# Kernel tuning notes

Measured on AMD Instinct MI355X. Metric: run time of the kernel, lower is better.

## Reference

```python
import jax, jax.numpy as jnp
import numpy as np

HEAD_DIM = 128
SCALE = 1.0 / np.sqrt(HEAD_DIM).astype(np.float32)


def setup_inputs() -> dict:
    key = jax.random.key(0)
    kq, kk, kv = jax.random.split(key, 3)
    B, S, H, KVH, D = 2, 2048, 32, 8, HEAD_DIM
    q = jax.random.normal(kq, (B, S, H, D), dtype=jnp.float32)
    k = jax.random.normal(kk, (B, S, KVH, D), dtype=jnp.float32)
    v = jax.random.normal(kv, (B, S, KVH, D), dtype=jnp.float32)
    return {"q": q, "k": k, "v": v}


def reference(q, k, v):
    # q: [B,S,H,D]; k,v: [B,S,KVH,D]
    B, S, H, D = q.shape
    kvh = k.shape[2]
    if kvh != H:
        rep = H // kvh
        # repeat_interleave along head dim (GQA -> MHA expansion)
        k = jnp.repeat(k, rep, axis=2)
        v = jnp.repeat(v, rep, axis=2)
    # scores: [B,H,S,S]
    scores = jnp.einsum("bqhd,bkhd->bhqk", q, k) * SCALE
    causal_mask = jnp.triu(jnp.ones((S, S), dtype=bool), k=1)
    scores = jnp.where(causal_mask, -jnp.inf, scores)
    attn = jax.nn.softmax(scores, axis=-1)
    # output back to [B,S,H,D]
    out = jnp.einsum("bhqk,bkhd->bqhd", attn, v)
    return out
```

## Files before the change

kernel.cpp:

```cpp
#include <hip/hip_runtime.h>
#include <hip/hip_bf16.h>
#include <stdint.h>

#define B_    2
#define S_    2048
#define H_    32
#define KVH_  8
#define D_    128
#define NBLK  256
#define NTOT_ 34

typedef __bf16 bf16x8 __attribute__((ext_vector_type(8)));
typedef unsigned short u16x8 __attribute__((ext_vector_type(8)));
typedef unsigned int u32x4 __attribute__((ext_vector_type(4)));
typedef float f32x16 __attribute__((ext_vector_type(16)));

__device__ constexpr float SCALE_LOG2E = 0.08838834764831845f * 1.4426950408889634f;

__device__ __forceinline__ unsigned short f2bf(float f) {
    unsigned int u = __builtin_bit_cast(unsigned int, f);
    u = (u + 0x7FFFu + ((u >> 16) & 1u)) >> 16;
    return (unsigned short)u;
}

__device__ __forceinline__ unsigned int cvt_pk_bf16(float lo, float hi) {
    unsigned int r;
    asm("v_cvt_pk_bf16_f32 %0, %1, %2" : "=v"(r) : "v"(lo), "v"(hi));
    return r;
}

__device__ __forceinline__ void gload16(const unsigned short* gsrc, unsigned short* ldst) {
    __builtin_amdgcn_global_load_lds(
        (const __attribute__((address_space(1))) unsigned int*)gsrc,
        (__attribute__((address_space(3))) unsigned int*)ldst,
        16, 0, 0);
}

__global__ __launch_bounds__(256) void prepass(const float* __restrict__ k,
                                               const float* __restrict__ v,
                                               unsigned short* __restrict__ kbuf,
                                               unsigned short* __restrict__ vbuf) {
    if (blockIdx.x < 1024) {
        __shared__ float tile[32][133];
        int bid = blockIdx.x;
        int kt  = bid & 63;
        int kvh = (bid >> 6) & 7;
        int b   = bid >> 9;
        int t   = threadIdx.x;

        #pragma unroll
        for (int i = 0; i < 4; ++i) {
            int idx = t + 256 * i;
            int r   = idx >> 5;
            int d4  = (idx & 31) * 4;
            float4 x = *(const float4*)(k + (((size_t)b * S_ + kt * 32 + r) * KVH_ + kvh) * D_ + d4);
            tile[r][d4 + 0] = x.x; tile[r][d4 + 1] = x.y;
            tile[r][d4 + 2] = x.z; tile[r][d4 + 3] = x.w;
        }
        __syncthreads();

        #pragma unroll
        for (int i = 0; i < 2; ++i) {
            int s2 = t + 256 * i;
            int ch = s2 >> 6;
            int l  = s2 & 63;
            int row = l & 31, d0 = ch * 16 + (l >> 5) * 8;
            u16x8 o;
            #pragma unroll
            for (int j = 0; j < 8; ++j) o[j] = f2bf(tile[row][d0 + j]);
            *(u16x8*)(kbuf + ((size_t)(((b * KVH_ + kvh) * 64 + kt) * 8 + ch) * 512 + l * 8)) = o;
        }
    } else {
        __shared__ float tile[64][132];
        int bid = blockIdx.x - 1024;
        int u   = bid & 31;
        int kvh = (bid >> 5) & 7;
        int b   = bid >> 8;
        int t   = threadIdx.x;

        int s  = t >> 2;
        int cb = (t & 3) * 32;
        const float* src = v + (((size_t)b * S_ + u * 64 + s) * KVH_ + kvh) * D_ + cb;
        #pragma unroll
        for (int i = 0; i < 8; ++i) {
            float4 x = ((const float4*)src)[i];
            tile[s][cb + 4 * i + 0] = x.x; tile[s][cb + 4 * i + 1] = x.y;
            tile[s][cb + 4 * i + 2] = x.z; tile[s][cb + 4 * i + 3] = x.w;
        }
        __syncthreads();

        #pragma unroll
        for (int i = 0; i < 4; ++i) {
            int slot = t + 256 * i;
            int ci = slot >> 6;
            int l  = slot & 63;
            int kk = ci >> 2, dt = ci & 3;
            int h2 = l >> 5;
            u16x8 o;
            #pragma unroll
            for (int j = 0; j < 8; ++j)
                o[j] = f2bf(tile[kk * 16 + h2 * 8 + j][dt * 32 + (l & 31)]);
            *(u16x8*)(vbuf + ((size_t)(((b * KVH_ + kvh) * 32 + u) * 16 + ci) * 512 + l * 8)) = o;
        }
    }
}

__global__ __launch_bounds__(512, 2)
void attn_fwd(const float* __restrict__ q,
              const unsigned short* __restrict__ kbuf,
              const unsigned short* __restrict__ vbuf,
              float* __restrict__ out)
{
    int pid = blockIdx.x;
    int lid = (pid & 7) * (NBLK / 8) + (pid >> 3);
    int p    = lid & 7;
    int hp   = (lid >> 3) & 1;
    int bkvh = lid >> 4;
    int b    = bkvh >> 3, kvh = bkvh & 7;
    const int qtA = 15 - p;
    const int NTA = 2 * qtA + 2;
    const int qtB = p;

    const int tid = threadIdx.x, wave = tid >> 6, lane = tid & 63;
    const int cw = wave & 3;
    const int h  = kvh * 4 + hp * 2 + (wave >> 2);
    const int c32 = lane & 31, hi = lane >> 5;

    __shared__ __align__(16) unsigned short ldsK[2][8192];
    __shared__ __align__(16) unsigned short ldsV[2][8192];

    const unsigned short* kfb = kbuf + (size_t)(b * KVH_ + kvh) * (S_ * D_);
    const unsigned short* vfb = vbuf + (size_t)(b * KVH_ + kvh) * (S_ * D_);

    auto kvt = [&](int u) { return (u < NTA) ? u : (u - NTA); };
    auto stageK = [&](int u) {
        const unsigned short* ks = kfb + (size_t)kvt(u) * 8192;
        unsigned short* ld = &ldsK[u & 1][0];
        #pragma unroll
        for (int i = 0; i < 2; ++i) {
            int seg = wave * 2 + i;
            gload16(ks + seg * 512 + lane * 8, ld + seg * 512);
        }
    };
    auto stageV = [&](int u) {
        const unsigned short* vs = vfb + (size_t)kvt(u) * 8192;
        unsigned short* ld = &ldsV[u & 1][0];
        #pragma unroll
        for (int i = 0; i < 2; ++i) {
            int seg = wave * 2 + i;
            gload16(vs + seg * 512 + lane * 8, ld + seg * 512);
        }
    };

    stageK(0);
    asm volatile("s_waitcnt vmcnt(0)" ::: "memory");
    __builtin_amdgcn_s_barrier();
    asm volatile("" ::: "memory");

    auto run_tile = [&](int qt, int u0, int NT) {
        const int q0w = qt * 128 + cw * 32;

        bf16x8 qf[8];
        {
            const float* qp = q + ((size_t)b * S_ + q0w + c32) * (H_ * D_) + h * D_ + hi * 8;
            #pragma unroll
            for (int ch = 0; ch < 8; ++ch) {
                float4 a  = ((const float4*)(qp + ch * 16))[0];
                float4 bb = ((const float4*)(qp + ch * 16))[1];
                u16x8 tt;
                tt[0] = f2bf(a.x * SCALE_LOG2E);  tt[1] = f2bf(a.y * SCALE_LOG2E);
                tt[2] = f2bf(a.z * SCALE_LOG2E);  tt[3] = f2bf(a.w * SCALE_LOG2E);
                tt[4] = f2bf(bb.x * SCALE_LOG2E); tt[5] = f2bf(bb.y * SCALE_LOG2E);
                tt[6] = f2bf(bb.z * SCALE_LOG2E); tt[7] = f2bf(bb.w * SCALE_LOG2E);
                qf[ch] = __builtin_bit_cast(bf16x8, tt);
            }
        }

        f32x16 acc[4];
        #pragma unroll
        for (int dt = 0; dt < 4; ++dt)
            #pragma unroll
            for (int i = 0; i < 16; ++i) acc[dt][i] = 0.f;
        float lsum = 0.f;

        u32x4 pfA[4], pfB[4];

        auto body = [&](int u, int it, int NT_, u32x4 (&pfW)[4], u32x4 (&pfR)[4], int ODD) {
            if (u + 1 < NTOT_) stageK(u + 1);
            stageV(u);
            const int k0 = it * 64;
            const bool act  = (k0 <= q0w + 31);
            const bool pact = (it > 0) && (k0 - 64 <= q0w + 31);
            f32x16 sv[2];

            if (act) {
                #pragma unroll
                for (int kt = 0; kt < 2; ++kt)
                    #pragma unroll
                    for (int i = 0; i < 16; ++i) sv[kt][i] = 0.f;
                __builtin_amdgcn_s_setprio(1);
                #pragma unroll
                for (int ch = 0; ch < 8; ++ch) {
                    bf16x8 kf0 = *(const bf16x8*)&ldsK[ODD][(0 * 8 + ch) * 512 + lane * 8];
                    bf16x8 kf1 = *(const bf16x8*)&ldsK[ODD][(1 * 8 + ch) * 512 + lane * 8];
                    sv[0] = __builtin_amdgcn_mfma_f32_32x32x16_bf16(kf0, qf[ch], sv[0], 0, 0, 0);
                    sv[1] = __builtin_amdgcn_mfma_f32_32x32x16_bf16(kf1, qf[ch], sv[1], 0, 0, 0);
                }
                __builtin_amdgcn_s_setprio(0);
            }

            if (pact) {
                __builtin_amdgcn_s_setprio(1);
                #pragma unroll
                for (int kk = 0; kk < 4; ++kk) {
                    bf16x8 pb = __builtin_bit_cast(bf16x8, pfR[kk]);
                    #pragma unroll
                    for (int dt = 0; dt < 4; ++dt) {
                        bf16x8 vf = *(const bf16x8*)&ldsV[ODD ^ 1][(kk * 4 + dt) * 512 + lane * 8];
                        acc[dt] = __builtin_amdgcn_mfma_f32_32x32x16_bf16(vf, pb, acc[dt], 0, 0, 0);
                    }
                }
                __builtin_amdgcn_s_setprio(0);
            }

            if (act) {
                if (k0 + 63 > q0w) {
                    #pragma unroll
                    for (int kt = 0; kt < 2; ++kt)
                        #pragma unroll
                        for (int r = 0; r < 16; ++r) {
                            int key = k0 + 32 * kt + (r & 3) + 8 * (r >> 2) + 4 * hi;
                            if (key > q0w + c32) sv[kt][r] = -INFINITY;
                        }
                }

                float pp[2][16];
                float sacc = 0.f;
                #pragma unroll
                for (int kt = 0; kt < 2; ++kt)
                    #pragma unroll
                    for (int r = 0; r < 16; ++r) {
                        pp[kt][r] = exp2f(sv[kt][r]);
                        sacc += pp[kt][r];
                    }
                lsum += sacc;

                #pragma unroll
                for (int kt = 0; kt < 2; ++kt) {
                    #pragma unroll
                    for (int kap = 0; kap < 2; ++kap) {
                        int base = kap * 8;
                        unsigned int U0 = cvt_pk_bf16(pp[kt][base + 0], pp[kt][base + 1]);
                        unsigned int U1 = cvt_pk_bf16(pp[kt][base + 2], pp[kt][base + 3]);
                        unsigned int V0 = cvt_pk_bf16(pp[kt][base + 4], pp[kt][base + 5]);
                        unsigned int V1 = cvt_pk_bf16(pp[kt][base + 6], pp[kt][base + 7]);
                        asm volatile("v_permlane32_swap_b32 %0, %1" : "+v"(U0), "+v"(V0));
                        asm volatile("v_permlane32_swap_b32 %0, %1" : "+v"(U1), "+v"(V1));
                        u32x4 W;
                        W[0] = U0;
                        W[1] = U1;
                        W[2] = V0;
                        W[3] = V1;
                        pfW[kt * 2 + kap] = W;
                    }
                }
            }

            asm volatile("s_waitcnt vmcnt(0)" ::: "memory");
            __builtin_amdgcn_s_barrier();
            asm volatile("" ::: "memory");
        };

        for (int it = 0; it < NT; it += 2) {
            body(u0 + it,     it,     NT, pfA, pfB, 0);
            body(u0 + it + 1, it + 1, NT, pfB, pfA, 1);
        }

        if (cw >= 2) {
            #pragma unroll
            for (int kk = 0; kk < 4; ++kk) {
                bf16x8 pb = __builtin_bit_cast(bf16x8, pfB[kk]);
                #pragma unroll
                for (int dt = 0; dt < 4; ++dt) {
                    bf16x8 vf = *(const bf16x8*)&ldsV[1][(kk * 4 + dt) * 512 + lane * 8];
                    acc[dt] = __builtin_amdgcn_mfma_f32_32x32x16_bf16(vf, pb, acc[dt], 0, 0, 0);
                }
            }
        }

        lsum += __shfl_xor(lsum, 32);
        float linv = 1.0f / lsum;
        float* ob = out + ((size_t)b * S_ + q0w + c32) * (H_ * D_) + h * D_;
        #pragma unroll
        for (int dt = 0; dt < 4; ++dt)
            #pragma unroll
            for (int rq = 0; rq < 4; ++rq) {
                float4 o;
                o.x = acc[dt][4 * rq + 0] * linv;
                o.y = acc[dt][4 * rq + 1] * linv;
                o.z = acc[dt][4 * rq + 2] * linv;
                o.w = acc[dt][4 * rq + 3] * linv;
                *(float4*)(ob + dt * 32 + rq * 8 + hi * 4) = o;
            }
    };

    run_tile(qtA, 0, NTA);
    run_tile(qtB, NTA, NTOT_ - NTA);
}

extern "C" void kernel_launch(void* const* d_in, const int* in_sizes, int n_in,
                              void* d_out, int out_size, void* d_ws, size_t ws_size,
                              hipStream_t stream) {
    const float* q = (const float*)d_in[0];
    const float* k = (const float*)d_in[1];
    const float* v = (const float*)d_in[2];
    float* out = (float*)d_out;

    unsigned short* kbuf = (unsigned short*)d_ws;
    unsigned short* vbuf = kbuf + (size_t)B_ * KVH_ * S_ * D_;

    prepass<<<1536, 256, 0, stream>>>(k, v, kbuf, vbuf);
    attn_fwd<<<NBLK, 512, 0, stream>>>(q, kbuf, vbuf, out);
}
```

Before: 111.2 us.

## Use 128-key KV tiles with immediate PV, drop software-pipelined P buffering

Each iteration now stages a 128-key block of K and V together, up from 64 keys with K and V staggered, which halves the number of barriers and iterations. QK and PV are done in the same iteration rather than deferring PV to the next step. LDS use doubles to 128KB, and the launch bounds no longer request two blocks per CU, so occupancy probably falls to one 512-thread block per CU. It also gives up the overlap the old schedule had between the QK MFMAs of one tile and the PV MFMAs of the previous tile.

```diff
diff --git a/kernel.cpp b/kernel.cpp
--- a/kernel.cpp
+++ b/kernel.cpp
@@ -8,7 +8,7 @@
 #define KVH_  8
 #define D_    128
 #define NBLK  256
-#define NTOT_ 34
+#define NTOT_ 17
 
 typedef __bf16 bf16x8 __attribute__((ext_vector_type(8)));
 typedef unsigned short u16x8 __attribute__((ext_vector_type(8)));
@@ -105,7 +105,7 @@
     }
 }
 
-__global__ __launch_bounds__(512, 2)
+__global__ __launch_bounds__(512)
 void attn_fwd(const float* __restrict__ q,
               const unsigned short* __restrict__ kbuf,
               const unsigned short* __restrict__ vbuf,
@@ -118,7 +118,7 @@
     int bkvh = lid >> 4;
     int b    = bkvh >> 3, kvh = bkvh & 7;
     const int qtA = 15 - p;
-    const int NTA = 2 * qtA + 2;
+    const int NTA = qtA + 1;
     const int qtB = p;
 
     const int tid = threadIdx.x, wave = tid >> 6, lane = tid & 63;
@@ -126,33 +126,28 @@
     const int h  = kvh * 4 + hp * 2 + (wave >> 2);
     const int c32 = lane & 31, hi = lane >> 5;
 
-    __shared__ __align__(16) unsigned short ldsK[2][8192];
-    __shared__ __align__(16) unsigned short ldsV[2][8192];
+    __shared__ __align__(16) unsigned short ldsK[2][16384];
+    __shared__ __align__(16) unsigned short ldsV[2][16384];
 
     const unsigned short* kfb = kbuf + (size_t)(b * KVH_ + kvh) * (S_ * D_);
     const unsigned short* vfb = vbuf + (size_t)(b * KVH_ + kvh) * (S_ * D_);
 
     auto kvt = [&](int u) { return (u < NTA) ? u : (u - NTA); };
-    auto stageK = [&](int u) {
-        const unsigned short* ks = kfb + (size_t)kvt(u) * 8192;
-        unsigned short* ld = &ldsK[u & 1][0];
-        #pragma unroll
-        for (int i = 0; i < 2; ++i) {
-            int seg = wave * 2 + i;
-            gload16(ks + seg * 512 + lane * 8, ld + seg * 512);
+    auto stagePair = [&](int u) {
+        const size_t off = (size_t)kvt(u) * 16384;
+        const unsigned short* ks = kfb + off;
+        const unsigned short* vs = vfb + off;
+        unsigned short* ldK = &ldsK[u & 1][0];
+        unsigned short* ldV = &ldsV[u & 1][0];
+        #pragma unroll
+        for (int i = 0; i < 4; ++i) {
+            int seg = wave * 4 + i;
+            gload16(ks + seg * 512 + lane * 8, ldK + seg * 512);
+            gload16(vs + seg * 512 + lane * 8, ldV + seg * 512);
         }
     };
-    auto stageV = [&](int u) {
-        const unsigned short* vs = vfb + (size_t)kvt(u) * 8192;
-        unsigned short* ld = &ldsV[u & 1][0];
-        #pragma unroll
-        for (int i = 0; i < 2; ++i) {
-            int seg = wave * 2 + i;
-            gload16(vs + seg * 512 + lane * 8, ld + seg * 512);
-        }
-    };
-
-    stageK(0);
+
+    stagePair(0);
     asm volatile("s_waitcnt vmcnt(0)" ::: "memory");
     __builtin_amdgcn_s_barrier();
     asm volatile("" ::: "memory");
@@ -183,57 +178,51 @@
             for (int i = 0; i < 16; ++i) acc[dt][i] = 0.f;
         float lsum = 0.f;
 
-        u32x4 pfA[4], pfB[4];
-
-        auto body = [&](int u, int it, int NT_, u32x4 (&pfW)[4], u32x4 (&pfR)[4], int ODD) {
-            if (u + 1 < NTOT_) stageK(u + 1);
-            stageV(u);
-            const int k0 = it * 64;
-            const bool act  = (k0 <= q0w + 31);
-            const bool pact = (it > 0) && (k0 - 64 <= q0w + 31);
-            f32x16 sv[2];
-
-            if (act) {
-                #pragma unroll
-                for (int kt = 0; kt < 2; ++kt)
-                    #pragma unroll
-                    for (int i = 0; i < 16; ++i) sv[kt][i] = 0.f;
-                __builtin_amdgcn_s_setprio(1);
+        for (int it = 0; it < NT; ++it) {
+            const int u = u0 + it;
+            if (u + 1 < NTOT_) stagePair(u + 1);
+            const unsigned short* ldK = &ldsK[u & 1][0];
+            const unsigned short* ldV = &ldsV[u & 1][0];
+            const bool diag  = (it == qt);
+            const bool s1act = (!diag) || (cw >= 2);
+
+            f32x16 sv0[2], sv1[2];
+            #pragma unroll
+            for (int kt = 0; kt < 2; ++kt)
+                #pragma unroll
+                for (int i = 0; i < 16; ++i) { sv0[kt][i] = 0.f; sv1[kt][i] = 0.f; }
+            __builtin_amdgcn_s_setprio(1);
+            #pragma unroll
+            for (int ch = 0; ch < 8; ++ch) {
+                bf16x8 k0 = *(const bf16x8*)&ldK[(0 * 8 + ch) * 512 + lane * 8];
+                bf16x8 k1 = *(const bf16x8*)&ldK[(1 * 8 + ch) * 512 + lane * 8];
+                sv0[0] = __builtin_amdgcn_mfma_f32_32x32x16_bf16(k0, qf[ch], sv0[0], 0, 0, 0);
+                sv0[1] = __builtin_amdgcn_mfma_f32_32x32x16_bf16(k1, qf[ch], sv0[1], 0, 0, 0);
+            }
+            if (s1act) {
                 #pragma unroll
                 for (int ch = 0; ch < 8; ++ch) {
-                    bf16x8 kf0 = *(const bf16x8*)&ldsK[ODD][(0 * 8 + ch) * 512 + lane * 8];
-                    bf16x8 kf1 = *(const bf16x8*)&ldsK[ODD][(1 * 8 + ch) * 512 + lane * 8];
-                    sv[0] = __builtin_amdgcn_mfma_f32_32x32x16_bf16(kf0, qf[ch], sv[0], 0, 0, 0);
-                    sv[1] = __builtin_amdgcn_mfma_f32_32x32x16_bf16(kf1, qf[ch], sv[1], 0, 0, 0);
+                    bf16x8 k2 = *(const bf16x8*)&ldK[(2 * 8 + ch) * 512 + lane * 8];
+                    bf16x8 k3 = *(const bf16x8*)&ldK[(3 * 8 + ch) * 512 + lane * 8];
+                    sv1[0] = __builtin_amdgcn_mfma_f32_32x32x16_bf16(k2, qf[ch], sv1[0], 0, 0, 0);
+                    sv1[1] = __builtin_amdgcn_mfma_f32_32x32x16_bf16(k3, qf[ch], sv1[1], 0, 0, 0);
                 }
-                __builtin_amdgcn_s_setprio(0);
-            }
-
-            if (pact) {
-                __builtin_amdgcn_s_setprio(1);
-                #pragma unroll
-                for (int kk = 0; kk < 4; ++kk) {
-                    bf16x8 pb = __builtin_bit_cast(bf16x8, pfR[kk]);
-                    #pragma unroll
-                    for (int dt = 0; dt < 4; ++dt) {
-                        bf16x8 vf = *(const bf16x8*)&ldsV[ODD ^ 1][(kk * 4 + dt) * 512 + lane * 8];
-                        acc[dt] = __builtin_amdgcn_mfma_f32_32x32x16_bf16(vf, pb, acc[dt], 0, 0, 0);
-                    }
-                }
-                __builtin_amdgcn_s_setprio(0);
-            }
-
-            if (act) {
-                if (k0 + 63 > q0w) {
+            }
+            __builtin_amdgcn_s_setprio(0);
+
+            #pragma unroll
+            for (int s = 0; s < 2; ++s) {
+                if (s == 1 && !s1act) break;
+                f32x16* sv = (s == 0) ? sv0 : sv1;
+                if (diag) {
                     #pragma unroll
                     for (int kt = 0; kt < 2; ++kt)
                         #pragma unroll
                         for (int r = 0; r < 16; ++r) {
-                            int key = k0 + 32 * kt + (r & 3) + 8 * (r >> 2) + 4 * hi;
-                            if (key > q0w + c32) sv[kt][r] = -INFINITY;
+                            int koff = s * 64 + kt * 32 + (r & 3) + 8 * (r >> 2) + 4 * hi;
+                            if (koff > cw * 32 + c32) sv[kt][r] = -INFINITY;
                         }
                 }
-
                 float pp[2][16];
                 float sacc = 0.f;
                 #pragma unroll
@@ -245,6 +234,7 @@
                     }
                 lsum += sacc;
 
+                u32x4 pf[4];
                 #pragma unroll
                 for (int kt = 0; kt < 2; ++kt) {
                     #pragma unroll
@@ -257,35 +247,27 @@
                         asm volatile("v_permlane32_swap_b32 %0, %1" : "+v"(U0), "+v"(V0));
                         asm volatile("v_permlane32_swap_b32 %0, %1" : "+v"(U1), "+v"(V1));
                         u32x4 W;
-                        W[0] = U0;
-                        W[1] = U1;
-                        W[2] = V0;
-                        W[3] = V1;
-                        pfW[kt * 2 + kap] = W;
+                        W[0] = U0; W[1] = U1; W[2] = V0; W[3] = V1;
+                        pf[kt * 2 + kap] = W;
                     }
                 }
+
+                __builtin_amdgcn_s_setprio(1);
+                #pragma unroll
+                for (int kk = 0; kk < 4; ++kk) {
+                    bf16x8 pb = __builtin_bit_cast(bf16x8, pf[kk]);
+                    #pragma unroll
+                    for (int dt = 0; dt < 4; ++dt) {
+                        bf16x8 vf = *(const bf16x8*)&ldV[s * 8192 + (kk * 4 + dt) * 512 + lane * 8];
+                        acc[dt] = __builtin_amdgcn_mfma_f32_32x32x16_bf16(vf, pb, acc[dt], 0, 0, 0);
+                    }
+                }
+                __builtin_amdgcn_s_setprio(0);
             }
 
             asm volatile("s_waitcnt vmcnt(0)" ::: "memory");
             __builtin_amdgcn_s_barrier();
             asm volatile("" ::: "memory");
-        };
-
-        for (int it = 0; it < NT; it += 2) {
-            body(u0 + it,     it,     NT, pfA, pfB, 0);
-            body(u0 + it + 1, it + 1, NT, pfB, pfA, 1);
-        }
-
-        if (cw >= 2) {
-            #pragma unroll
-            for (int kk = 0; kk < 4; ++kk) {
-                bf16x8 pb = __builtin_bit_cast(bf16x8, pfB[kk]);
-                #pragma unroll
-                for (int dt = 0; dt < 4; ++dt) {
-                    bf16x8 vf = *(const bf16x8*)&ldsV[1][(kk * 4 + dt) * 512 + lane * 8];
-                    acc[dt] = __builtin_amdgcn_mfma_f32_32x32x16_bf16(vf, pb, acc[dt], 0, 0, 0);
-                }
-            }
         }
 
         lsum += __shfl_xor(lsum, 32);
```

After: 111.9 us. About the same (+0.6%).
